# Optimization experiments

Hardware: AMD Instinct MI355X
Metric: run time of the kernel (lower is better)

Reference implementation:

```python
import jax, jax.numpy as jnp
import numpy as np

N = 10000      # nodes
F_IN = 256     # input feature dim
H1 = 128       # hidden_dim1
H2 = 64        # hidden_dim2 (latent)
E = 320000     # edges (avg degree 32)


def setup_inputs() -> dict:
    key = jax.random.key(0)
    ks = jax.random.split(key, 10)
    x = jax.random.normal(ks[0], (N, F_IN), dtype=jnp.float32)
    edge_index = jax.random.randint(ks[1], (2, E), 0, N, dtype=jnp.int64)
    edge_weight = jax.random.uniform(ks[2], (E,), dtype=jnp.float32)
    s1 = 1.0 / np.sqrt(F_IN)
    s2 = 1.0 / np.sqrt(H1)
    W1 = jax.random.normal(ks[3], (F_IN, H1), dtype=jnp.float32) * s1
    b1 = jnp.zeros((H1,), dtype=jnp.float32)
    W2 = jax.random.normal(ks[4], (H1, H2), dtype=jnp.float32) * s2
    b2 = jnp.zeros((H2,), dtype=jnp.float32)
    W3 = jax.random.normal(ks[5], (H1, H2), dtype=jnp.float32) * s2
    b3 = jnp.zeros((H2,), dtype=jnp.float32)
    return {"x": x, "edge_index": edge_index, "edge_weight": edge_weight,
            "W1": W1, "b1": b1, "W2": W2, "b2": b2, "W3": W3, "b3": b3}


def _gcn_norm(edge_index, edge_weight, n):
    # add self-loops with weight 1, symmetric deg^-1/2 normalization (PyG GCNConv)
    loop = jnp.arange(n)
    row = jnp.concatenate([edge_index[0], loop])
    col = jnp.concatenate([edge_index[1], loop])
    w = jnp.concatenate([edge_weight, jnp.ones((n,), edge_weight.dtype)])
    deg = jax.ops.segment_sum(w, col, num_segments=n)
    dis = jnp.where(deg > 0, jax.lax.rsqrt(deg), 0.0)
    norm = dis[row] * w * dis[col]
    return row, col, norm


def _gcn_conv(h, W, b, row, col, norm, n):
    hw = h @ W                                   # [N, out] transform first (PyG order)
    out = jax.ops.segment_sum(norm[:, None] * hw[row], col, num_segments=n)
    return out + b


def reference(x, edge_index, edge_weight, W1, b1, W2, b2, W3, b3):
    n = x.shape[0]
    row, col, norm = _gcn_norm(edge_index, edge_weight, n)
    h1 = jax.nn.relu(_gcn_conv(x, W1, b1, row, col, norm, n))
    mu = _gcn_conv(h1, W2, b2, row, col, norm, n)
    logvar = _gcn_conv(h1, W3, b3, row, col, norm, n)
    # eval mode: reparameterize -> mu, dropout inactive, decoder act = identity
    z = mu
    adj = z @ z.T                                # [N, N] inner-product decode
    return adj, mu, logvar
```

## Files before the change

### kernel.cpp

```cpp
#include <hip/hip_runtime.h>

#define N_NODES 10000
#define F_IN    256
#define H1      128
#define H2      64
#define NEDGE   320000
#define M_TOT   (NEDGE + N_NODES)


__global__ void k_init(float* deg, int* cnt) {
    int i = blockIdx.x * blockDim.x + threadIdx.x;
    if (i < N_NODES) { deg[i] = 1.0f; cnt[i] = 1; }
}

__global__ void k_count(const int* __restrict__ ei, const float* __restrict__ w,
                        float* deg, int* cnt) {
    int e = blockIdx.x * blockDim.x + threadIdx.x;
    if (e < NEDGE) {
        int c = ei[NEDGE + e];
        atomicAdd(&deg[c], w[e]);
        atomicAdd(&cnt[c], 1);
    }
}

__global__ void k_rsqrt(float* deg) {
    int i = blockIdx.x * blockDim.x + threadIdx.x;
    if (i < N_NODES) deg[i] = rsqrtf(deg[i]);
}

__global__ void k_scan(const int* __restrict__ cnt, int* __restrict__ ptr,
                       int* __restrict__ cur) {
    __shared__ int part[1024];
    int t = threadIdx.x;
    int base = t * 10;
    int local[10];
    int s = 0;
#pragma unroll
    for (int j = 0; j < 10; j++) {
        int idx = base + j;
        int v = (idx < N_NODES) ? cnt[idx] : 0;
        local[j] = s;
        s += v;
    }
    part[t] = s;
    __syncthreads();
    for (int off = 1; off < 1024; off <<= 1) {
        int v = (t >= off) ? part[t - off] : 0;
        __syncthreads();
        part[t] += v;
        __syncthreads();
    }
    int excl = t ? part[t - 1] : 0;
#pragma unroll
    for (int j = 0; j < 10; j++) {
        int idx = base + j;
        if (idx < N_NODES) {
            int p = excl + local[j];
            ptr[idx] = p;
            cur[idx] = p;
        }
    }
    if (t == 1023) ptr[N_NODES] = part[1023];
}

__global__ void k_scatter(const int* __restrict__ ei, const float* __restrict__ w,
                          const float* __restrict__ dis, int* cur,
                          int* __restrict__ src, float* __restrict__ wgt) {
    int t = blockIdx.x * blockDim.x + threadIdx.x;
    if (t >= M_TOT) return;
    int r, c; float nw;
    if (t < NEDGE) {
        r = ei[t];
        c = ei[NEDGE + t];
        nw = dis[r] * w[t] * dis[c];
    } else {
        r = c = t - NEDGE;
        float d = dis[r];
        nw = d * d;
    }
    int pos = atomicAdd(&cur[c], 1);
    src[pos] = r;
    wgt[pos] = nw;
}


__global__ __launch_bounds__(128) void k_gemm1(const float* __restrict__ x,
                                               const float* __restrict__ W1,
                                               float* __restrict__ hw) {
    __shared__ float xs[8 * F_IN];
    int i0 = blockIdx.x * 8;
    int t = threadIdx.x;
    const float4* xsrc = (const float4*)(x + (size_t)i0 * F_IN);
    float4* xd = (float4*)xs;
#pragma unroll
    for (int j = 0; j < 4; j++) xd[t + j * 128] = xsrc[t + j * 128];
    __syncthreads();
    float acc[8] = {0, 0, 0, 0, 0, 0, 0, 0};
    for (int k = 0; k < F_IN; k++) {
        float wv = W1[k * H1 + t];
#pragma unroll
        for (int r = 0; r < 8; r++) acc[r] += xs[r * F_IN + k] * wv;
    }
#pragma unroll
    for (int r = 0; r < 8; r++) hw[(size_t)(i0 + r) * H1 + t] = acc[r];
}

__global__ __launch_bounds__(128) void k_gemm23(const float* __restrict__ h1,
                                                const float* __restrict__ W2,
                                                const float* __restrict__ W3,
                                                float* __restrict__ t2,
                                                float* __restrict__ t3) {
    __shared__ float hs[8 * H1];
    int i0 = blockIdx.x * 8;
    int t = threadIdx.x;
    const float4* hsrc = (const float4*)(h1 + (size_t)i0 * H1);
    float4* hd = (float4*)hs;
#pragma unroll
    for (int j = 0; j < 2; j++) hd[t + j * 128] = hsrc[t + j * 128];
    __syncthreads();
    int f = t & 63;
    int sel = t >> 6;
    const float* W = sel ? W3 : W2;
    float acc[8] = {0, 0, 0, 0, 0, 0, 0, 0};
    for (int k = 0; k < H1; k++) {
        float wv = W[k * H2 + f];
#pragma unroll
        for (int r = 0; r < 8; r++) acc[r] += hs[r * H1 + k] * wv;
    }
    float* o = sel ? t3 : t2;
#pragma unroll
    for (int r = 0; r < 8; r++) o[(size_t)(i0 + r) * H2 + f] = acc[r];
}


__global__ __launch_bounds__(128) void k_agg1(const int* __restrict__ ptr,
                                              const int* __restrict__ src,
                                              const float* __restrict__ wgt,
                                              const float* __restrict__ hw,
                                              const float* __restrict__ b1,
                                              float* __restrict__ h1) {
    int i = blockIdx.x;
    int f = threadIdx.x;
    int jb = ptr[i], je = ptr[i + 1];
    float acc = b1[f];
    for (int j = jb; j < je; j++)
        acc += wgt[j] * hw[(size_t)src[j] * H1 + f];
    h1[(size_t)i * H1 + f] = fmaxf(acc, 0.0f);
}

__global__ __launch_bounds__(128) void k_agg2(const int* __restrict__ ptr,
                                              const int* __restrict__ src,
                                              const float* __restrict__ wgt,
                                              const float* __restrict__ t2,
                                              const float* __restrict__ t3,
                                              const float* __restrict__ b2,
                                              const float* __restrict__ b3,
                                              float* __restrict__ mu,
                                              float* __restrict__ lv) {
    int i = blockIdx.x;
    int t = threadIdx.x;
    int f = t & 63;
    int sel = t >> 6;
    const float* tin = sel ? t3 : t2;
    float acc = sel ? b3[f] : b2[f];
    int jb = ptr[i], je = ptr[i + 1];
    for (int j = jb; j < je; j++)
        acc += wgt[j] * tin[(size_t)src[j] * H2 + f];
    float* o = sel ? lv : mu;
    o[(size_t)i * H2 + f] = acc;
}


__global__ __launch_bounds__(256) void k_adj(const float* __restrict__ z,
                                             float* __restrict__ adj) {
    __shared__ float As[64][128];
    __shared__ float Bs[64][128];
    int tid = threadIdx.x;
    int tx = tid & 15, ty = tid >> 4;
    int rowBase = blockIdx.y * 128, colBase = blockIdx.x * 128;

    int m = tid >> 1;
    int kh = (tid & 1) * 32;
    {
        int gr = rowBase + m;
        const float4* zr = (const float4*)(z + (size_t)gr * H2 + kh);
#pragma unroll
        for (int q = 0; q < 8; q++) {
            float4 v = make_float4(0.f, 0.f, 0.f, 0.f);
            if (gr < N_NODES) v = zr[q];
            int k = kh + q * 4;
            As[k][m] = v.x; As[k + 1][m] = v.y; As[k + 2][m] = v.z; As[k + 3][m] = v.w;
        }
        int gc = colBase + m;
        const float4* zc = (const float4*)(z + (size_t)gc * H2 + kh);
#pragma unroll
        for (int q = 0; q < 8; q++) {
            float4 v = make_float4(0.f, 0.f, 0.f, 0.f);
            if (gc < N_NODES) v = zc[q];
            int k = kh + q * 4;
            Bs[k][m] = v.x; Bs[k + 1][m] = v.y; Bs[k + 2][m] = v.z; Bs[k + 3][m] = v.w;
        }
    }
    __syncthreads();

    float acc[8][8];
#pragma unroll
    for (int i = 0; i < 8; i++)
#pragma unroll
        for (int j = 0; j < 8; j++) acc[i][j] = 0.f;

    for (int k = 0; k < 64; k++) {
        float4 a0 = *(const float4*)&As[k][ty * 4];
        float4 a1 = *(const float4*)&As[k][ty * 4 + 64];
        float4 b0 = *(const float4*)&Bs[k][tx * 4];
        float4 b1v = *(const float4*)&Bs[k][tx * 4 + 64];
        float a[8] = {a0.x, a0.y, a0.z, a0.w, a1.x, a1.y, a1.z, a1.w};
        float b[8] = {b0.x, b0.y, b0.z, b0.w, b1v.x, b1v.y, b1v.z, b1v.w};
#pragma unroll
        for (int i = 0; i < 8; i++)
#pragma unroll
            for (int j = 0; j < 8; j++) acc[i][j] += a[i] * b[j];
    }

#pragma unroll
    for (int i = 0; i < 8; i++) {
        int rm = rowBase + ty * 4 + ((i < 4) ? i : 64 + (i - 4));
        if (rm >= N_NODES) continue;
        float* orow = adj + (size_t)rm * N_NODES;
        int c0 = colBase + tx * 4;
        if (c0 < N_NODES)
            *(float4*)&orow[c0] = make_float4(acc[i][0], acc[i][1], acc[i][2], acc[i][3]);
        int c1 = c0 + 64;
        if (c1 < N_NODES)
            *(float4*)&orow[c1] = make_float4(acc[i][4], acc[i][5], acc[i][6], acc[i][7]);
    }
}


extern "C" void kernel_launch(void* const* d_in, const int* in_sizes, int n_in,
                              void* d_out, int out_size, void* d_ws, size_t ws_size,
                              hipStream_t stream) {
    const float* x  = (const float*)d_in[0];
    const int*   ei = (const int*)d_in[1];
    const float* w  = (const float*)d_in[2];
    const float* W1 = (const float*)d_in[3];
    const float* b1 = (const float*)d_in[4];
    const float* W2 = (const float*)d_in[5];
    const float* b2 = (const float*)d_in[6];
    const float* W3 = (const float*)d_in[7];
    const float* b3 = (const float*)d_in[8];

    float* out = (float*)d_out;
    float* adj = out;
    float* mu  = out + (size_t)N_NODES * N_NODES;
    float* lv  = mu + (size_t)N_NODES * H2;

    float* ws  = out + 80000000;
    float* deg = ws;
    int*   cnt = (int*)(ws + 10240);
    int*   ptr = (int*)(ws + 20480);
    int*   cur = (int*)(ws + 30720);
    int*   src = (int*)(ws + 40960);
    float* wgt = ws + 371200;
    float* hw  = ws + 701440;
    float* h1  = ws + 1981440;
    float* t2  = ws + 3261440;
    float* t3  = ws + 3901440;

    hipLaunchKernelGGL(k_init,    dim3((N_NODES + 255) / 256), dim3(256), 0, stream, deg, cnt);
    hipLaunchKernelGGL(k_count,   dim3((NEDGE + 255) / 256),   dim3(256), 0, stream, ei, w, deg, cnt);
    hipLaunchKernelGGL(k_rsqrt,   dim3((N_NODES + 255) / 256), dim3(256), 0, stream, deg);
    hipLaunchKernelGGL(k_scan,    dim3(1), dim3(1024), 0, stream, cnt, ptr, cur);
    hipLaunchKernelGGL(k_scatter, dim3((M_TOT + 255) / 256),   dim3(256), 0, stream, ei, w, deg, cur, src, wgt);
    hipLaunchKernelGGL(k_gemm1,   dim3(N_NODES / 8),  dim3(128), 0, stream, x, W1, hw);
    hipLaunchKernelGGL(k_agg1,    dim3(N_NODES),      dim3(128), 0, stream, ptr, src, wgt, hw, b1, h1);
    hipLaunchKernelGGL(k_gemm23,  dim3(N_NODES / 8),  dim3(128), 0, stream, h1, W2, W3, t2, t3);
    hipLaunchKernelGGL(k_agg2,    dim3(N_NODES),      dim3(128), 0, stream, ptr, src, wgt, t2, t3, b2, b3, mu, lv);

    dim3 g((N_NODES + 127) / 128, (N_NODES + 127) / 128);
    hipLaunchKernelGGL(k_adj, g, dim3(256), 0, stream, mu, adj);
}
```

Baseline: 720.8 us.

## Use split-bf16 MFMA for adjacency decode, fuse rsqrt, unroll small GEMMs

The adjacency outer product z·zᵀ moves from a scalar FP32 register-tiled kernel to MFMA bf16 instructions. Each float is split into three bf16 parts (high, mid, low), and six cross-product MFMAs are summed to recover near-FP32 accuracy. The A/B tiles go into XOR-swizzled shared memory, and the K loop is split into two stages that overlap partially. The separate rsqrt kernel is folded into the scatter kernel. The two small GEMM inner loops are unrolled by four using float4 shared-memory reads. The accuracy loss from the truncated split is a risk, and the output stores become scalar with a column-major fragment pattern, which may be less coalesced than the previous float4 stores on this write-bound kernel.

```diff
diff --git a/kernel.cpp b/kernel.cpp
--- a/kernel.cpp
+++ b/kernel.cpp
@@ -6,6 +6,10 @@
 #define H2      64
 #define NEDGE   320000
 #define M_TOT   (NEDGE + N_NODES)
+
+typedef __attribute__((ext_vector_type(8))) short          s16v8;
+typedef __attribute__((ext_vector_type(8))) unsigned short u16v8;
+typedef __attribute__((ext_vector_type(4))) float          f32v4;
 
 
 __global__ void k_init(float* deg, int* cnt) {
@@ -23,11 +27,6 @@
     }
 }
 
-__global__ void k_rsqrt(float* deg) {
-    int i = blockIdx.x * blockDim.x + threadIdx.x;
-    if (i < N_NODES) deg[i] = rsqrtf(deg[i]);
-}
-
 __global__ void k_scan(const int* __restrict__ cnt, int* __restrict__ ptr,
                        int* __restrict__ cur) {
     __shared__ int part[1024];
@@ -64,7 +63,7 @@
 }
 
 __global__ void k_scatter(const int* __restrict__ ei, const float* __restrict__ w,
-                          const float* __restrict__ dis, int* cur,
+                          const float* __restrict__ deg, int* cur,
                           int* __restrict__ src, float* __restrict__ wgt) {
     int t = blockIdx.x * blockDim.x + threadIdx.x;
     if (t >= M_TOT) return;
@@ -72,10 +71,10 @@
     if (t < NEDGE) {
         r = ei[t];
         c = ei[NEDGE + t];
-        nw = dis[r] * w[t] * dis[c];
+        nw = rsqrtf(deg[r]) * w[t] * rsqrtf(deg[c]);
     } else {
         r = c = t - NEDGE;
-        float d = dis[r];
+        float d = rsqrtf(deg[r]);
         nw = d * d;
     }
     int pos = atomicAdd(&cur[c], 1);
@@ -96,10 +95,16 @@
     for (int j = 0; j < 4; j++) xd[t + j * 128] = xsrc[t + j * 128];
     __syncthreads();
     float acc[8] = {0, 0, 0, 0, 0, 0, 0, 0};
-    for (int k = 0; k < F_IN; k++) {
-        float wv = W1[k * H1 + t];
-#pragma unroll
-        for (int r = 0; r < 8; r++) acc[r] += xs[r * F_IN + k] * wv;
+    for (int k = 0; k < F_IN; k += 4) {
+        float w0 = W1[(k + 0) * H1 + t];
+        float w1 = W1[(k + 1) * H1 + t];
+        float w2 = W1[(k + 2) * H1 + t];
+        float w3 = W1[(k + 3) * H1 + t];
+#pragma unroll
+        for (int r = 0; r < 8; r++) {
+            float4 xv = *(const float4*)&xs[r * F_IN + k];
+            acc[r] += xv.x * w0 + xv.y * w1 + xv.z * w2 + xv.w * w3;
+        }
     }
 #pragma unroll
     for (int r = 0; r < 8; r++) hw[(size_t)(i0 + r) * H1 + t] = acc[r];
@@ -122,10 +127,16 @@
     int sel = t >> 6;
     const float* W = sel ? W3 : W2;
     float acc[8] = {0, 0, 0, 0, 0, 0, 0, 0};
-    for (int k = 0; k < H1; k++) {
-        float wv = W[k * H2 + f];
-#pragma unroll
-        for (int r = 0; r < 8; r++) acc[r] += hs[r * H1 + k] * wv;
+    for (int k = 0; k < H1; k += 4) {
+        float w0 = W[(k + 0) * H2 + f];
+        float w1 = W[(k + 1) * H2 + f];
+        float w2 = W[(k + 2) * H2 + f];
+        float w3 = W[(k + 3) * H2 + f];
+#pragma unroll
+        for (int r = 0; r < 8; r++) {
+            float4 hv = *(const float4*)&hs[r * H1 + k];
+            acc[r] += hv.x * w0 + hv.y * w1 + hv.z * w2 + hv.w * w3;
+        }
     }
     float* o = sel ? t3 : t2;
 #pragma unroll
@@ -170,69 +181,136 @@
     o[(size_t)i * H2 + f] = acc;
 }
 
-
-__global__ __launch_bounds__(256) void k_adj(const float* __restrict__ z,
-                                             float* __restrict__ adj) {
-    __shared__ float As[64][128];
-    __shared__ float Bs[64][128];
+__global__ __launch_bounds__(256, 1) void k_adj(const float* __restrict__ z,
+                                                float* __restrict__ adj) {
+    __shared__ __align__(16) unsigned short Ap[3][128 * 32];
+    __shared__ __align__(16) unsigned short Bp[3][128 * 32];
     int tid = threadIdx.x;
-    int tx = tid & 15, ty = tid >> 4;
     int rowBase = blockIdx.y * 128, colBase = blockIdx.x * 128;
 
-    int m = tid >> 1;
-    int kh = (tid & 1) * 32;
-    {
-        int gr = rowBase + m;
-        const float4* zr = (const float4*)(z + (size_t)gr * H2 + kh);
-#pragma unroll
-        for (int q = 0; q < 8; q++) {
-            float4 v = make_float4(0.f, 0.f, 0.f, 0.f);
-            if (gr < N_NODES) v = zr[q];
-            int k = kh + q * 4;
-            As[k][m] = v.x; As[k + 1][m] = v.y; As[k + 2][m] = v.z; As[k + 3][m] = v.w;
-        }
-        int gc = colBase + m;
-        const float4* zc = (const float4*)(z + (size_t)gc * H2 + kh);
-#pragma unroll
-        for (int q = 0; q < 8; q++) {
-            float4 v = make_float4(0.f, 0.f, 0.f, 0.f);
-            if (gc < N_NODES) v = zc[q];
-            int k = kh + q * 4;
-            Bs[k][m] = v.x; Bs[k + 1][m] = v.y; Bs[k + 2][m] = v.z; Bs[k + 3][m] = v.w;
-        }
-    }
-    __syncthreads();
-
-    float acc[8][8];
-#pragma unroll
-    for (int i = 0; i < 8; i++)
-#pragma unroll
-        for (int j = 0; j < 8; j++) acc[i][j] = 0.f;
-
-    for (int k = 0; k < 64; k++) {
-        float4 a0 = *(const float4*)&As[k][ty * 4];
-        float4 a1 = *(const float4*)&As[k][ty * 4 + 64];
-        float4 b0 = *(const float4*)&Bs[k][tx * 4];
-        float4 b1v = *(const float4*)&Bs[k][tx * 4 + 64];
-        float a[8] = {a0.x, a0.y, a0.z, a0.w, a1.x, a1.y, a1.z, a1.w};
-        float b[8] = {b0.x, b0.y, b0.z, b0.w, b1v.x, b1v.y, b1v.z, b1v.w};
-#pragma unroll
-        for (int i = 0; i < 8; i++)
-#pragma unroll
-            for (int j = 0; j < 8; j++) acc[i][j] += a[i] * b[j];
-    }
-
-#pragma unroll
-    for (int i = 0; i < 8; i++) {
-        int rm = rowBase + ty * 4 + ((i < 4) ? i : 64 + (i - 4));
-        if (rm >= N_NODES) continue;
-        float* orow = adj + (size_t)rm * N_NODES;
-        int c0 = colBase + tx * 4;
-        if (c0 < N_NODES)
-            *(float4*)&orow[c0] = make_float4(acc[i][0], acc[i][1], acc[i][2], acc[i][3]);
-        int c1 = c0 + 64;
-        if (c1 < N_NODES)
-            *(float4*)&orow[c1] = make_float4(acc[i][4], acc[i][5], acc[i][6], acc[i][7]);
+    int lane = tid & 63;
+    int wv   = tid >> 6;
+    int wr = (wv >> 1) * 64;
+    int wc = (wv & 1) * 64;
+    int lrow = lane & 15;
+    int lk   = lane >> 4;
+
+    int sr   = tid & 127;
+    int isB  = tid >> 7;
+    int gbase = (isB ? colBase : rowBase) + sr;
+    bool ok = gbase < N_NODES;
+    const float* srcp = z + (size_t)gbase * 64;
+    unsigned short* P0 = isB ? Bp[0] : Ap[0];
+    unsigned short* P1 = isB ? Bp[1] : Ap[1];
+    unsigned short* P2 = isB ? Bp[2] : Ap[2];
+
+    auto stage = [&](int s) {
+#pragma unroll
+        for (int g = 0; g < 4; g++) {
+            float v[8];
+            if (ok) {
+                float4 a = *(const float4*)(srcp + s * 32 + g * 8);
+                float4 b = *(const float4*)(srcp + s * 32 + g * 8 + 4);
+                v[0] = a.x; v[1] = a.y; v[2] = a.z; v[3] = a.w;
+                v[4] = b.x; v[5] = b.y; v[6] = b.z; v[7] = b.w;
+            } else {
+#pragma unroll
+                for (int q = 0; q < 8; q++) v[q] = 0.0f;
+            }
+            u16v8 hv, mv, lv8;
+#pragma unroll
+            for (int q = 0; q < 8; q++) {
+                float xv = v[q];
+                unsigned hu = __float_as_uint(xv) & 0xffff0000u;
+                float r1 = xv - __uint_as_float(hu);
+                unsigned mu2 = __float_as_uint(r1) & 0xffff0000u;
+                float r2 = r1 - __uint_as_float(mu2);
+                unsigned lu = __float_as_uint(r2) & 0xffff0000u;
+                hv[q]  = (unsigned short)(hu >> 16);
+                mv[q]  = (unsigned short)(mu2 >> 16);
+                lv8[q] = (unsigned short)(lu >> 16);
+            }
+            int c = g ^ ((sr >> 1) & 3);
+            int idx = sr * 32 + c * 8;
+            *reinterpret_cast<u16v8*>(P0 + idx) = hv;
+            *reinterpret_cast<u16v8*>(P1 + idx) = mv;
+            *reinterpret_cast<u16v8*>(P2 + idx) = lv8;
+        }
+    };
+
+    f32v4 acc[4][4];
+#pragma unroll
+    for (int i = 0; i < 4; i++)
+#pragma unroll
+        for (int j = 0; j < 4; j++) acc[i][j] = (f32v4)0.0f;
+
+    s16v8 a0[4], a1[4], a2[4], b0[4], b1[4], b2[4];
+
+#define LOADFRAGS()                                                        \
+    {                                                                      \
+        _Pragma("unroll")                                                  \
+        for (int fq = 0; fq < 4; fq++) {                                   \
+            int ra = wr + fq * 16 + lrow;                                  \
+            int ca = lk ^ ((ra >> 1) & 3);                                 \
+            int ia = ra * 32 + ca * 8;                                     \
+            a0[fq] = *reinterpret_cast<const s16v8*>(&Ap[0][ia]);          \
+            a1[fq] = *reinterpret_cast<const s16v8*>(&Ap[1][ia]);          \
+            a2[fq] = *reinterpret_cast<const s16v8*>(&Ap[2][ia]);          \
+            int rb = wc + fq * 16 + lrow;                                  \
+            int cb = lk ^ ((rb >> 1) & 3);                                 \
+            int ib = rb * 32 + cb * 8;                                     \
+            b0[fq] = *reinterpret_cast<const s16v8*>(&Bp[0][ib]);          \
+            b1[fq] = *reinterpret_cast<const s16v8*>(&Bp[1][ib]);          \
+            b2[fq] = *reinterpret_cast<const s16v8*>(&Bp[2][ib]);          \
+        }                                                                  \
+    }
+
+#define MFMAS()                                                            \
+    {                                                                      \
+        _Pragma("unroll")                                                  \
+        for (int i = 0; i < 4; i++) {                                      \
+            _Pragma("unroll")                                              \
+            for (int j = 0; j < 4; j++) {                                  \
+                f32v4 c = acc[i][j];                                       \
+                c = __builtin_amdgcn_mfma_f32_16x16x32_bf16(a0[i], b0[j], c, 0, 0, 0); \
+                c = __builtin_amdgcn_mfma_f32_16x16x32_bf16(a0[i], b1[j], c, 0, 0, 0); \
+                c = __builtin_amdgcn_mfma_f32_16x16x32_bf16(a1[i], b0[j], c, 0, 0, 0); \
+                c = __builtin_amdgcn_mfma_f32_16x16x32_bf16(a0[i], b2[j], c, 0, 0, 0); \
+                c = __builtin_amdgcn_mfma_f32_16x16x32_bf16(a2[i], b0[j], c, 0, 0, 0); \
+                c = __builtin_amdgcn_mfma_f32_16x16x32_bf16(a1[i], b1[j], c, 0, 0, 0); \
+                acc[i][j] = c;                                             \
+            }                                                              \
+        }                                                                  \
+    }
+
+    stage(0);
+    __syncthreads();
+    LOADFRAGS();
+    __syncthreads();
+    stage(1);
+    MFMAS();
+    __syncthreads();
+    LOADFRAGS();
+    MFMAS();
+
+#undef LOADFRAGS
+#undef MFMAS
+
+#pragma unroll
+    for (int i = 0; i < 4; i++) {
+        int r0 = rowBase + wr + i * 16 + lk * 4;
+#pragma unroll
+        for (int j = 0; j < 4; j++) {
+            int cg = colBase + wc + j * 16 + lrow;
+            if (cg < N_NODES) {
+#pragma unroll
+                for (int v = 0; v < 4; v++) {
+                    int rg = r0 + v;
+                    if (rg < N_NODES)
+                        adj[(size_t)rg * N_NODES + cg] = acc[i][j][v];
+                }
+            }
+        }
     }
 }
 
@@ -269,7 +347,6 @@
 
     hipLaunchKernelGGL(k_init,    dim3((N_NODES + 255) / 256), dim3(256), 0, stream, deg, cnt);
     hipLaunchKernelGGL(k_count,   dim3((NEDGE + 255) / 256),   dim3(256), 0, stream, ei, w, deg, cnt);
-    hipLaunchKernelGGL(k_rsqrt,   dim3((N_NODES + 255) / 256), dim3(256), 0, stream, deg);
     hipLaunchKernelGGL(k_scan,    dim3(1), dim3(1024), 0, stream, cnt, ptr, cur);
     hipLaunchKernelGGL(k_scatter, dim3((M_TOT + 255) / 256),   dim3(256), 0, stream, ei, w, deg, cur, src, wgt);
     hipLaunchKernelGGL(k_gemm1,   dim3(N_NODES / 8),  dim3(128), 0, stream, x, W1, hw);
```

After: 666.8 us. -7.5%, faster.
